# Kernel optimization log

Measured on AMD Instinct MI355X. Metric: run time of the kernel, lower is better.

The kernel has to match this reference:

```python
import jax, jax.numpy as jnp
import numpy as np

NUM_CLASS = 20
STRIDE = 4.0
B, H, W, G, NV = 8, 128, 128, 64, 40


def setup_inputs() -> dict:
    key = jax.random.key(0)
    ks = jax.random.split(key, 8)
    keypoints = jax.random.normal(ks[0], (B, H, W, NUM_CLASS), jnp.float32)
    preg = jax.random.uniform(ks[1], (B, H, W, 4), jnp.float32, 1.0, 40.0)
    fpn = jax.random.normal(ks[2], (B, H, W, NUM_CLASS), jnp.float32)
    masks = jnp.ones((B, H, W, G), jnp.float32)
    scalar_y = jax.random.uniform(ks[3], (B, G), jnp.float32, 5.0, 25.0)
    scalar_x = jax.random.uniform(ks[4], (B, G), jnp.float32, 5.0, 25.0)
    # ground truth: [cy, cx, y1, x1, y2, x2, class]; rows >= NV are zero padding
    rng = np.random.default_rng(0)
    gt = np.zeros((B, G, 7), np.float32)
    cy = rng.uniform(20.0, 492.0, (B, NV)).astype(np.float32)
    cx = rng.uniform(20.0, 492.0, (B, NV)).astype(np.float32)
    hh = rng.uniform(16.0, 120.0, (B, NV)).astype(np.float32)
    ww = rng.uniform(16.0, 120.0, (B, NV)).astype(np.float32)
    gt[:, :NV, 0] = cy
    gt[:, :NV, 1] = cx
    gt[:, :NV, 2] = np.clip(cy - hh / 2, 1.0, 510.0)
    gt[:, :NV, 3] = np.clip(cx - ww / 2, 1.0, 510.0)
    gt[:, :NV, 4] = np.clip(cy + hh / 2, 1.0, 510.0)
    gt[:, :NV, 5] = np.clip(cx + ww / 2, 1.0, 510.0)
    gt[:, :NV, 6] = rng.integers(1, NUM_CLASS + 1, (B, NV)).astype(np.float32)
    return {
        "keypoints": keypoints,
        "preg": preg,
        "fpn": fpn,
        "ground_truth": jnp.asarray(gt),
        "masks": masks,
        "scalar_y": scalar_y,
        "scalar_x": scalar_x,
    }


def _image_loss(gravity_pred, dist_pred, heatmap_pred, gt, masks, sy, sx):
    f32 = jnp.float32
    Hh, Ww, C = gravity_pred.shape
    Gg = gt.shape[0]
    # padding boundary: first row whose cy (col 0) is the minimum (==0 padding)
    slice_index = jnp.argmin(gt[:, 0])
    valid = jnp.arange(Gg) < slice_index
    vf = valid.astype(f32)

    gy = (gt[:, 0] + 0.5) / STRIDE
    gx = (gt[:, 1] + 0.5) / STRIDE
    by1 = (gt[:, 2] + 0.5) / STRIDE
    bx1 = (gt[:, 3] + 0.5) / STRIDE
    by2 = (gt[:, 4] + 0.5) / STRIDE
    bx2 = (gt[:, 5] + 0.5) / STRIDE
    cid = gt[:, 6].astype(jnp.int32) - 1
    kp_y = jnp.clip(jnp.floor(gt[:, 0] / STRIDE).astype(jnp.int32), 0, Hh - 1)
    kp_x = jnp.clip(jnp.floor(gt[:, 1] / STRIDE).astype(jnp.int32), 0, Ww - 1)

    grid_y = (jnp.arange(Hh, dtype=f32) + 0.5)[:, None, None]  # [H,1,1]
    grid_x = (jnp.arange(Ww, dtype=f32) + 0.5)[None, :, None]  # [1,W,1]

    dist_l = grid_x - bx1  # [1,W,G]
    dist_r = bx2 - grid_x
    dist_t = grid_y - by1  # [H,1,G]
    dist_b = by2 - grid_y
    ymask = (dist_t > 0.0).astype(f32) * (dist_b > 0.0).astype(f32)
    xmask = (dist_l > 0.0).astype(f32) * (dist_r > 0.0).astype(f32)
    heatmask = ymask * xmask * masks * vf  # [H,W,G]
    dist_l = dist_l * heatmask
    dist_r = dist_r * heatmask
    dist_t = dist_t * heatmask
    dist_b = dist_b * heatmask
    loc = jnp.max(heatmask, axis=-1)  # [H,W]
    dist_area = (dist_l + dist_r) * (dist_t + dist_b)
    area_pad = dist_area + (1.0 - heatmask) * 1e8
    area_min = jnp.min(area_pad, axis=-1, keepdims=True)
    dist_mask = (dist_area == area_min).astype(f32) * loc[..., None]  # [H,W,G]
    dl = jnp.max(dist_l * dist_mask, axis=-1)
    dr = jnp.max(dist_r * dist_mask, axis=-1)
    dt = jnp.max(dist_t * dist_mask, axis=-1)
    db = jnp.max(dist_b * dist_mask, axis=-1)

    pl, pr, pt, pb = (dist_pred[..., k] for k in range(4))
    inter = (jnp.minimum(dl, pl) + jnp.minimum(dr, pr)) * (jnp.minimum(dt, pt) + jnp.minimum(db, pb))
    union = (dl + dr) * (dt + db) + (pl + pr) * (pt + pb) - inter
    iou = inter / (union + 1e-12)

    red = jnp.exp(-(((grid_y - 0.5 - jnp.floor(gy)) / jnp.sqrt(sy)) ** 2
                    + ((grid_x - 0.5 - jnp.floor(gx)) / jnp.sqrt(sx)) ** 2) / 2.0) * vf  # [H,W,G]
    iou_red = jnp.max(red, axis=-1)
    iou_loss = jnp.sum(-jnp.log(iou + 1e-12) * loc * (iou_red * 4.0 + 1.0))

    # per-class max over gts of that class (== boolean_mask + reduce_max; empty -> 0)
    seg = jnp.where(valid & (cid >= 0) & (cid < C), cid, C)
    red_gt = jnp.maximum(jax.ops.segment_max(red.transpose(2, 0, 1), seg, num_segments=C + 1)[:C], 0.0).transpose(1, 2, 0)
    hm_gt = jnp.maximum(jax.ops.segment_max(dist_mask.transpose(2, 0, 1), seg, num_segments=C + 1)[:C], 0.0).transpose(1, 2, 0)
    gt_kp = jnp.zeros((Hh, Ww, C + 1), f32).at[kp_y, kp_x, seg].max(vf)[..., :C]

    sig, ls = jax.nn.sigmoid, jax.nn.log_sigmoid
    pos = -(1.0 - sig(gravity_pred)) ** 2 * ls(gravity_pred) * gt_kp
    neg = -(1.0 - red_gt) ** 4 * sig(gravity_pred) ** 2 * (-gravity_pred + ls(gravity_pred)) * (1.0 - gt_kp)
    gravity_loss = jnp.sum(pos) + jnp.sum(neg)

    hpos = -10.0 * (1.0 - sig(heatmap_pred)) ** 2 * ls(heatmap_pred) * hm_gt
    hneg = -10.0 * sig(heatmap_pred) ** 2 * (-heatmap_pred + ls(heatmap_pred)) * (1.0 - hm_gt)
    s_hg = jnp.sum(hm_gt)
    hm_loss = jnp.sum(hneg) / (jnp.asarray(Hh * Ww * C, f32) - s_hg)

    cond = s_hg != 0.0
    safe_hg = jnp.where(cond, s_hg, 1.0)
    s_loc = jnp.sum(loc)
    safe_loc = jnp.where(s_loc > 0.0, s_loc, 1.0)
    n_valid = jnp.maximum(slice_index.astype(f32), 1.0)
    hm2 = hm_loss + jnp.sum(hpos) / safe_hg
    iou_out = jnp.where(cond, iou_loss / safe_loc, 0.0)
    grav_out = jnp.where(cond, gravity_loss / n_valid, 0.0)
    hm_out = jnp.where(cond, hm2, hm_loss)
    total = jnp.where(cond, iou_out + grav_out + hm2, hm_loss)
    return iou_out, hm_out, grav_out, total


def reference(keypoints, preg, fpn, ground_truth, masks, scalar_y, scalar_x):
    losses = jax.vmap(_image_loss)(keypoints, preg, fpn, ground_truth, masks, scalar_y, scalar_x)
    # layer returns the mean total loss over the batch
    return jnp.mean(losses[3])
```

## Files before the change

### kernel.cpp

```cpp
#include <hip/hip_runtime.h>
#include <math.h>

#define Bc 8
#define Hc 128
#define Wc 128
#define Cc 20
#define Gc 64
#define HWc (Hc*Wc)
#define NBLK (Bc*HWc/256)

#define WS_STRIDE 768
#define OFF_BOX   0
#define OFF_RED   256
#define OFF_KPIX  512
#define OFF_SEG   576
#define OFF_START 640
#define WS_NV     704
#define WS_ACC    705
#define WS_SLICE  712

__global__ __launch_bounds__(64) void prep_kernel(
    const float* __restrict__ gt, const float* __restrict__ sy,
    const float* __restrict__ sx, float* __restrict__ ws)
{
  const int b = blockIdx.x;
  const int g = threadIdx.x;
  const float* row = gt + (size_t)(b*Gc + g)*7;
  const float cy = row[0];
  const float cx = row[1];

  float v = cy; int idx = g;
  #pragma unroll
  for (int o = 32; o > 0; o >>= 1) {
    const float ov = __shfl_down(v, o, 64);
    const int   oi = __shfl_down(idx, o, 64);
    if (ov < v || (ov == v && oi < idx)) { v = ov; idx = oi; }
  }
  const int slice = __shfl(idx, 0, 64);
  const bool valid = g < slice;
  const int cid = (int)row[6] - 1;
  const int cls = (cid >= 0 && cid < Cc) ? cid : Cc;

  __shared__ int counts[Cc+1], offs[Cc+1], starts[Cc+2];
  if (g < Cc+1) { counts[g] = 0; offs[g] = 0; }
  __syncthreads();
  if (valid) atomicAdd(&counts[cls], 1);
  __syncthreads();
  if (g == 0) {
    int acc = 0;
    for (int c = 0; c < Cc+1; ++c) { starts[c] = acc; acc += counts[c]; }
    starts[Cc+1] = acc;
  }
  __syncthreads();

  float* wb = ws + (size_t)b*WS_STRIDE;
  int*  wbi = (int*)wb;
  float4 bx;
  bx.x = (row[2]+0.5f)*0.25f;
  bx.y = (row[3]+0.5f)*0.25f;
  bx.z = (row[4]+0.5f)*0.25f;
  bx.w = (row[5]+0.5f)*0.25f;
  ((float4*)(wb + OFF_BOX))[g] = bx;
  wbi[OFF_SEG+g] = (valid && cls < Cc) ? cls : Cc;
  if (valid) {
    const int pos = starts[cls] + atomicAdd(&offs[cls], 1);
    float4 rp;
    rp.x = floorf((cy+0.5f)*0.25f);
    rp.y = floorf((cx+0.5f)*0.25f);
    rp.z = 0.5f / sy[b*Gc+g];
    rp.w = 0.5f / sx[b*Gc+g];
    ((float4*)(wb + OFF_RED))[pos] = rp;
    int kpy = (int)floorf(cy*0.25f); kpy = kpy < 0 ? 0 : (kpy > Hc-1 ? Hc-1 : kpy);
    int kpx = (int)floorf(cx*0.25f); kpx = kpx < 0 ? 0 : (kpx > Wc-1 ? Wc-1 : kpx);
    wbi[OFF_KPIX+pos] = kpy*Wc + kpx;
  }
  if (g < Cc+2) wbi[OFF_START+g] = starts[g];
  if (g == 0) { wb[WS_NV] = fmaxf((float)slice, 1.0f); wbi[WS_SLICE] = slice; }
  if (g < 6) wb[WS_ACC+g] = 0.0f;
}

__device__ __forceinline__ float wave_sum(float v) {
  #pragma unroll
  for (int o = 32; o > 0; o >>= 1) v += __shfl_down(v, o, 64);
  return v;
}

__global__ __launch_bounds__(256, 4) void main_kernel(
  const float* __restrict__ kpt, const float* __restrict__ preg,
  const float* __restrict__ fpn, const float* __restrict__ masks,
  const float* __restrict__ wsc, float* __restrict__ wsa)
{
  __shared__ float s_part[4][6];

  const int tid = threadIdx.x;
  const int b   = blockIdx.x >> 6;
  const int pix = blockIdx.x*256 + tid;
  const int hw  = pix & (HWc-1);
  const int h = hw >> 7, w = hw & (Wc-1);

  const float* wb  = wsc + (size_t)b*WS_STRIDE;
  const int*   wbi = (const int*)wb;
  const float4* __restrict__ box4 = (const float4*)(wb + OFF_BOX);
  const float4* __restrict__ red4 = (const float4*)(wb + OFF_RED);
  const int nslice = wbi[WS_SLICE];

  const float wx = w + 0.5f, hy = h + 0.5f;
  const float px_ = (float)w, py_ = (float)h;
  const float4* mrow4 = (const float4*)(masks + (size_t)pix*Gc);

  float amin = 3.0e38f; float loc = 0.0f, mmin = 0.0f; int gmin = 0;
  const int nfull = nslice & ~7;
  float4 ma = mrow4[0], mb = mrow4[1];
  for (int g0 = 0; g0 < nfull; g0 += 8) {
    const int pf = (g0 + 8) < Gc ? ((g0 + 8) >> 2) : 14;
    const float4 na = mrow4[pf];
    const float4 nb = mrow4[pf + 1];
    #pragma unroll
    for (int j = 0; j < 8; ++j) {
      const int g = g0 + j;
      const float m = (j==0)?ma.x:(j==1)?ma.y:(j==2)?ma.z:(j==3)?ma.w
                    : (j==4)?mb.x:(j==5)?mb.y:(j==6)?mb.z:mb.w;
      const float4 bx = box4[g];
      const float dl = wx - bx.y, dr = bx.w - wx;
      const float dt = hy - bx.x, db = bx.z - hy;
      const bool inb = (dl > 0.f) & (dr > 0.f) & (dt > 0.f) & (db > 0.f);
      const float hm = inb ? m : 0.f;
      const float area = (dl*hm + dr*hm) * (dt*hm + db*hm);
      const float ap = area + (1.f - hm)*1e8f;
      if (ap < amin) { amin = ap; gmin = g; mmin = m; }
      loc = fmaxf(loc, hm);
    }
    ma = na; mb = nb;
  }
  for (int g = nfull; g < nslice; ++g) {
    const float m = masks[(size_t)pix*Gc + g];
    const float4 bx = box4[g];
    const float dl = wx - bx.y, dr = bx.w - wx;
    const float dt = hy - bx.x, db = bx.z - hy;
    const bool inb = (dl > 0.f) & (dr > 0.f) & (dt > 0.f) & (db > 0.f);
    const float hm = inb ? m : 0.f;
    const float area = (dl*hm + dr*hm) * (dt*hm + db*hm);
    const float ap = area + (1.f - hm)*1e8f;
    if (ap < amin) { amin = ap; gmin = g; mmin = m; }
    loc = fmaxf(loc, hm);
  }

  float dlm=0.f, drm=0.f, dtm=0.f, dbm=0.f, hmval=0.f; int cmin = Cc;
  if (loc > 0.f) {
    const float4 bx = box4[gmin];
    const float dl = wx - bx.y, dr = bx.w - wx;
    const float dt = hy - bx.x, db = bx.z - hy;
    const float area = (dl*mmin + dr*mmin) * (dt*mmin + db*mmin);
    if (area == amin) {
      dlm = dl*mmin*loc; drm = dr*mmin*loc; dtm = dt*mmin*loc; dbm = db*mmin*loc;
      cmin = wbi[OFF_SEG + gmin];
      hmval = loc;
    }
  }

  const float4* kq4 = (const float4*)(kpt + (size_t)pix*Cc);
  const float4* fq4 = (const float4*)(fpn + (size_t)pix*Cc);
  float4 kcur = kq4[0], fcur = fq4[0];
  float gargmax = -1e30f, grav = 0.f, hneg = 0.f;
  int sb = wbi[OFF_START];
  for (int cg = 0; cg < 5; ++cg) {
    const int nx = cg < 4 ? cg + 1 : 4;
    const float4 knxt = kq4[nx];
    const float4 fnxt = fq4[nx];
    #pragma unroll
    for (int j = 0; j < 4; ++j) {
      const int c = cg*4 + j;
      const int s1 = wbi[OFF_START + c + 1];
      float ramax = -1e30f; bool kpv = false;
      for (int i = sb; i < s1; ++i) {
        const float4 rp = red4[i];
        const int kpix = wbi[OFF_KPIX + i];
        const float dy = py_ - rp.x, dx = px_ - rp.y;
        const float arg = -(dy*dy*rp.z + dx*dx*rp.w);
        ramax = fmaxf(ramax, arg);
        kpv = kpv | (kpix == hw);
      }
      sb = s1;
      const float rmax = __expf(ramax);
      gargmax = fmaxf(gargmax, ramax);
      const float x  = (j==0)?kcur.x:(j==1)?kcur.y:(j==2)?kcur.z:kcur.w;
      const float e  = __expf(-fabsf(x));
      const float t  = 1.f + e;
      const float r  = 1.f / t;
      const float L  = __logf(t);
      const float s  = (x >= 0.f) ? r : e*r;
      const float lsx = fminf(x, 0.f) - L;
      const float kv = kpv ? 1.f : 0.f;
      const float om = 1.f - rmax;
      const float om4 = (om*om)*(om*om);
      const float oms = 1.f - s;
      grav += (-(oms*oms)*lsx)*kv + (-om4*(s*s)*(lsx - x))*(1.f - kv);

      const float fx  = (j==0)?fcur.x:(j==1)?fcur.y:(j==2)?fcur.z:fcur.w;
      const float ef  = __expf(-fabsf(fx));
      const float tf  = 1.f + ef;
      const float rf  = 1.f / tf;
      const float Lf  = __logf(tf);
      const float sf  = (fx >= 0.f) ? rf : ef*rf;
      const float lsf = fminf(fx, 0.f) - Lf;
      hneg += -10.f*(sf*sf)*(lsf - fx);
    }
    kcur = knxt; fcur = fnxt;
  }
  {
    const int e20 = wbi[OFF_START + Cc + 1];
    for (int i = sb; i < e20; ++i) {
      const float4 rp = red4[i];
      const float dy = py_ - rp.x, dx = px_ - rp.y;
      gargmax = fmaxf(gargmax, -(dy*dy*rp.z + dx*dx*rp.w));
    }
  }
  const float iou_red = __expf(gargmax);

  const float4 p4 = *(const float4*)(preg + (size_t)pix*4);
  const float inter = (fminf(dlm,p4.x)+fminf(drm,p4.y)) * (fminf(dtm,p4.z)+fminf(dbm,p4.w));
  const float uni = (dlm+drm)*(dtm+dbm) + (p4.x+p4.y)*(p4.z+p4.w) - inter;
  const float iou = inter / (uni + 1e-12f);
  const float t_iou = -__logf(iou + 1e-12f) * loc * (iou_red*4.f + 1.f);

  float hpos = 0.f, shg = 0.f;
  if (hmval > 0.f && cmin < Cc) {
    const float fx  = fpn[(size_t)pix*Cc + cmin];
    const float ef  = __expf(-fabsf(fx));
    const float tf  = 1.f + ef;
    const float rf  = 1.f / tf;
    const float Lf  = __logf(tf);
    const float sf  = (fx >= 0.f) ? rf : ef*rf;
    const float lsf = fminf(fx, 0.f) - Lf;
    const float osf = 1.f - sf;
    hpos = -10.f*(osf*osf)*lsf*hmval;
    hneg -= (-10.f*(sf*sf)*(lsf - fx))*hmval;
    shg = hmval;
  }

  float v0 = wave_sum(t_iou);
  float v1 = wave_sum(loc);
  float v2 = wave_sum(grav);
  float v3 = wave_sum(hpos);
  float v4 = wave_sum(hneg);
  float v5 = wave_sum(shg);
  const int wv = tid >> 6, ln = tid & 63;
  if (ln == 0) {
    s_part[wv][0]=v0; s_part[wv][1]=v1; s_part[wv][2]=v2;
    s_part[wv][3]=v3; s_part[wv][4]=v4; s_part[wv][5]=v5;
  }
  __syncthreads();
  if (tid < 6) {
    const float a = s_part[0][tid] + s_part[1][tid] + s_part[2][tid] + s_part[3][tid];
    atomicAdd(wsa + (size_t)b*WS_STRIDE + WS_ACC + tid, a);
  }
}

__global__ __launch_bounds__(64) void fin_kernel(const float* __restrict__ ws,
                                                 float* __restrict__ out)
{
  const int b = threadIdx.x;
  float total = 0.0f;
  if (b < Bc) {
    const float* wb = ws + (size_t)b*WS_STRIDE;
    const float iou_loss = wb[WS_ACC+0];
    const float s_loc    = wb[WS_ACC+1];
    const float grav     = wb[WS_ACC+2];
    const float hposs    = wb[WS_ACC+3];
    const float hnegs    = wb[WS_ACC+4];
    const float shg      = wb[WS_ACC+5];
    const float nv       = wb[WS_NV];
    const float hm_loss  = hnegs / ((float)(HWc*Cc) - shg);
    const bool  cond     = (shg != 0.0f);
    const float safe_hg  = cond ? shg : 1.0f;
    const float safe_loc = (s_loc > 0.0f) ? s_loc : 1.0f;
    const float hm2      = hm_loss + hposs/safe_hg;
    total = cond ? (iou_loss/safe_loc + grav/nv + hm2) : hm_loss;
  }
  #pragma unroll
  for (int o = 4; o > 0; o >>= 1) total += __shfl_down(total, o, 64);
  if (b == 0) out[0] = total * (1.0f/(float)Bc);
}

extern "C" void kernel_launch(void* const* d_in, const int* in_sizes, int n_in,
                              void* d_out, int out_size, void* d_ws, size_t ws_size,
                              hipStream_t stream) {
  const float* kpt  = (const float*)d_in[0];
  const float* preg = (const float*)d_in[1];
  const float* fpn  = (const float*)d_in[2];
  const float* gt   = (const float*)d_in[3];
  const float* mk   = (const float*)d_in[4];
  const float* sy   = (const float*)d_in[5];
  const float* sx   = (const float*)d_in[6];
  float* ws  = (float*)d_ws;
  float* out = (float*)d_out;

  prep_kernel<<<Bc, 64, 0, stream>>>(gt, sy, sx, ws);
  main_kernel<<<NBLK, 256, 0, stream>>>(kpt, preg, fpn, mk, ws, ws);
  fin_kernel<<<1, 64, 0, stream>>>(ws, out);
}
```

Baseline: 116.6 us.

## Fuse prep into main kernel, stage inputs via coalesced LDS transposes, drop atomics

Removes the separate prep kernel: each main block recomputes the per-image GT slice, class buckets and gaussian parameters in shared memory. Keypoint, fpn and mask rows are loaded with coalesced block-wide float4 reads and transposed through LDS, with masks streamed in 16-group chunks and the next chunk prefetched into registers. Per-block partial sums are written to the workspace and reduced in a widened final kernel instead of using global atomics. This costs about 45KB of LDS per block, lowers the occupancy hint to 2, adds extra barriers, and repeats the GT prep work in every block.

```diff
diff --git a/kernel.cpp b/kernel.cpp
--- a/kernel.cpp
+++ b/kernel.cpp
@@ -9,75 +9,6 @@
 #define HWc (Hc*Wc)
 #define NBLK (Bc*HWc/256)
 
-#define WS_STRIDE 768
-#define OFF_BOX   0
-#define OFF_RED   256
-#define OFF_KPIX  512
-#define OFF_SEG   576
-#define OFF_START 640
-#define WS_NV     704
-#define WS_ACC    705
-#define WS_SLICE  712
-
-__global__ __launch_bounds__(64) void prep_kernel(
-    const float* __restrict__ gt, const float* __restrict__ sy,
-    const float* __restrict__ sx, float* __restrict__ ws)
-{
-  const int b = blockIdx.x;
-  const int g = threadIdx.x;
-  const float* row = gt + (size_t)(b*Gc + g)*7;
-  const float cy = row[0];
-  const float cx = row[1];
-
-  float v = cy; int idx = g;
-  #pragma unroll
-  for (int o = 32; o > 0; o >>= 1) {
-    const float ov = __shfl_down(v, o, 64);
-    const int   oi = __shfl_down(idx, o, 64);
-    if (ov < v || (ov == v && oi < idx)) { v = ov; idx = oi; }
-  }
-  const int slice = __shfl(idx, 0, 64);
-  const bool valid = g < slice;
-  const int cid = (int)row[6] - 1;
-  const int cls = (cid >= 0 && cid < Cc) ? cid : Cc;
-
-  __shared__ int counts[Cc+1], offs[Cc+1], starts[Cc+2];
-  if (g < Cc+1) { counts[g] = 0; offs[g] = 0; }
-  __syncthreads();
-  if (valid) atomicAdd(&counts[cls], 1);
-  __syncthreads();
-  if (g == 0) {
-    int acc = 0;
-    for (int c = 0; c < Cc+1; ++c) { starts[c] = acc; acc += counts[c]; }
-    starts[Cc+1] = acc;
-  }
-  __syncthreads();
-
-  float* wb = ws + (size_t)b*WS_STRIDE;
-  int*  wbi = (int*)wb;
-  float4 bx;
-  bx.x = (row[2]+0.5f)*0.25f;
-  bx.y = (row[3]+0.5f)*0.25f;
-  bx.z = (row[4]+0.5f)*0.25f;
-  bx.w = (row[5]+0.5f)*0.25f;
-  ((float4*)(wb + OFF_BOX))[g] = bx;
-  wbi[OFF_SEG+g] = (valid && cls < Cc) ? cls : Cc;
-  if (valid) {
-    const int pos = starts[cls] + atomicAdd(&offs[cls], 1);
-    float4 rp;
-    rp.x = floorf((cy+0.5f)*0.25f);
-    rp.y = floorf((cx+0.5f)*0.25f);
-    rp.z = 0.5f / sy[b*Gc+g];
-    rp.w = 0.5f / sx[b*Gc+g];
-    ((float4*)(wb + OFF_RED))[pos] = rp;
-    int kpy = (int)floorf(cy*0.25f); kpy = kpy < 0 ? 0 : (kpy > Hc-1 ? Hc-1 : kpy);
-    int kpx = (int)floorf(cx*0.25f); kpx = kpx < 0 ? 0 : (kpx > Wc-1 ? Wc-1 : kpx);
-    wbi[OFF_KPIX+pos] = kpy*Wc + kpx;
-  }
-  if (g < Cc+2) wbi[OFF_START+g] = starts[g];
-  if (g == 0) { wb[WS_NV] = fmaxf((float)slice, 1.0f); wbi[WS_SLICE] = slice; }
-  if (g < 6) wb[WS_ACC+g] = 0.0f;
-}
 
 __device__ __forceinline__ float wave_sum(float v) {
   #pragma unroll
@@ -85,44 +16,128 @@
   return v;
 }
 
-__global__ __launch_bounds__(256, 4) void main_kernel(
-  const float* __restrict__ kpt, const float* __restrict__ preg,
-  const float* __restrict__ fpn, const float* __restrict__ masks,
-  const float* __restrict__ wsc, float* __restrict__ wsa)
+__global__ __launch_bounds__(256, 2) void main_kernel(
+    const float* __restrict__ kpt, const float* __restrict__ preg,
+    const float* __restrict__ fpn, const float* __restrict__ masks,
+    const float* __restrict__ gt,  const float* __restrict__ sy,
+    const float* __restrict__ sx,  float* __restrict__ ws)
 {
+  __shared__ float s_kpt[Cc*256];
+  __shared__ float s_fpn[Cc*256];
+  __shared__ float s_masks[16*256];
+  __shared__ float4 s_red[Gc];
+  __shared__ int s_kpix[Gc];
+  __shared__ int s_seg[Gc];
+  __shared__ int s_starts[Cc+2];
+  __shared__ int s_counts[Cc+1];
+  __shared__ int s_offs[Cc+1];
+  __shared__ int s_nslice;
   __shared__ float s_part[4][6];
 
-  const int tid = threadIdx.x;
-  const int b   = blockIdx.x >> 6;
-  const int pix = blockIdx.x*256 + tid;
-  const int hw  = pix & (HWc-1);
+  const int T = threadIdx.x;
+  const int b = blockIdx.x >> 6;
+  const int pixbase = blockIdx.x * 256;
+  const int pix = pixbase + T;
+  const int hw = pix & (HWc-1);
   const int h = hw >> 7, w = hw & (Wc-1);
 
-  const float* wb  = wsc + (size_t)b*WS_STRIDE;
-  const int*   wbi = (const int*)wb;
-  const float4* __restrict__ box4 = (const float4*)(wb + OFF_BOX);
-  const float4* __restrict__ red4 = (const float4*)(wb + OFF_RED);
-  const int nslice = wbi[WS_SLICE];
+  const float4* __restrict__ kg4 = (const float4*)(kpt + (size_t)pixbase*Cc);
+  const float4* __restrict__ fg4 = (const float4*)(fpn + (size_t)pixbase*Cc);
+  const float4* __restrict__ mg4 = (const float4*)(masks + (size_t)pixbase*Gc);
+  float4 kpr[5], fpr[5], mpr[4];
+  #pragma unroll
+  for (int k = 0; k < 5; ++k) { kpr[k] = kg4[T + 256*k]; fpr[k] = fg4[T + 256*k]; }
+  #pragma unroll
+  for (int k = 0; k < 4; ++k) mpr[k] = mg4[((T>>2) + 64*k)*16 + (T&3)];
+
+  if (T < Cc+1) { s_counts[T] = 0; s_offs[T] = 0; }
+  float cy = 0.f, cx = 0.f; int cls = Cc; bool valid = false;
+  if (T < 64) {
+    const float* grow = gt + (size_t)(b*Gc + T)*7;
+    cy = grow[0]; cx = grow[1];
+    float v = cy; int idx = T;
+    #pragma unroll
+    for (int o = 32; o > 0; o >>= 1) {
+      const float ov = __shfl_down(v, o, 64);
+      const int   oi = __shfl_down(idx, o, 64);
+      if (ov < v || (ov == v && oi < idx)) { v = ov; idx = oi; }
+    }
+    const int slice = __shfl(idx, 0, 64);
+    const int cid = (int)grow[6] - 1;
+    cls = (cid >= 0 && cid < Cc) ? cid : Cc;
+    valid = T < slice;
+    s_seg[T] = (valid && cls < Cc) ? cls : Cc;
+    if (T == 0) s_nslice = slice;
+  }
+  __syncthreads();
+  if (T < 64 && valid) atomicAdd(&s_counts[cls], 1);
+  __syncthreads();
+  if (T == 0) {
+    int acc = 0;
+    #pragma unroll
+    for (int c = 0; c < Cc+1; ++c) { s_starts[c] = acc; acc += s_counts[c]; }
+    s_starts[Cc+1] = acc;
+  }
+  __syncthreads();
+  if (T < 64 && valid) {
+    const int pos = s_starts[cls] + atomicAdd(&s_offs[cls], 1);
+    float4 rp;
+    rp.x = floorf((cy + 0.5f)*0.25f);
+    rp.y = floorf((cx + 0.5f)*0.25f);
+    rp.z = 0.5f / sy[b*Gc + T];
+    rp.w = 0.5f / sx[b*Gc + T];
+    s_red[pos] = rp;
+    int kpy = (int)floorf(cy*0.25f); kpy = kpy < 0 ? 0 : (kpy > Hc-1 ? Hc-1 : kpy);
+    int kpx = (int)floorf(cx*0.25f); kpx = kpx < 0 ? 0 : (kpx > Wc-1 ? Wc-1 : kpx);
+    s_kpix[pos] = kpy*Wc + kpx;
+  }
+
+  #pragma unroll
+  for (int k = 0; k < 5; ++k) {
+    const int base = (T + 256*k)*4;
+    const float ke[4] = {kpr[k].x, kpr[k].y, kpr[k].z, kpr[k].w};
+    const float fe[4] = {fpr[k].x, fpr[k].y, fpr[k].z, fpr[k].w};
+    #pragma unroll
+    for (int i = 0; i < 4; ++i) {
+      const int li = base + i;
+      const int p = li / 20;
+      const int c = li - p*20;
+      s_kpt[c*256 + p] = ke[i];
+      s_fpn[c*256 + p] = fe[i];
+    }
+  }
+  #pragma unroll
+  for (int k = 0; k < 4; ++k) {
+    const int p  = (T>>2) + 64*k;
+    const int g0 = (T&3)*4;
+    const float me[4] = {mpr[k].x, mpr[k].y, mpr[k].z, mpr[k].w};
+    #pragma unroll
+    for (int i = 0; i < 4; ++i) s_masks[(g0+i)*256 + p] = me[i];
+  }
+  #pragma unroll
+  for (int k = 0; k < 4; ++k) mpr[k] = mg4[((T>>2) + 64*k)*16 + 4 + (T&3)];
+  __syncthreads();
+
+  const int nslice = s_nslice;
+  const int nch = (nslice + 15) >> 4;
 
   const float wx = w + 0.5f, hy = h + 0.5f;
+  const float wxp = wx - 0.125f, wxm = 0.125f - wx;
+  const float hyp = hy - 0.125f, hym = 0.125f - hy;
   const float px_ = (float)w, py_ = (float)h;
-  const float4* mrow4 = (const float4*)(masks + (size_t)pix*Gc);
-
-  float amin = 3.0e38f; float loc = 0.0f, mmin = 0.0f; int gmin = 0;
-  const int nfull = nslice & ~7;
-  float4 ma = mrow4[0], mb = mrow4[1];
-  for (int g0 = 0; g0 < nfull; g0 += 8) {
-    const int pf = (g0 + 8) < Gc ? ((g0 + 8) >> 2) : 14;
-    const float4 na = mrow4[pf];
-    const float4 nb = mrow4[pf + 1];
-    #pragma unroll
-    for (int j = 0; j < 8; ++j) {
-      const int g = g0 + j;
-      const float m = (j==0)?ma.x:(j==1)?ma.y:(j==2)?ma.z:(j==3)?ma.w
-                    : (j==4)?mb.x:(j==5)?mb.y:(j==6)?mb.z:mb.w;
-      const float4 bx = box4[g];
-      const float dl = wx - bx.y, dr = bx.w - wx;
-      const float dt = hy - bx.x, db = bx.z - hy;
+
+  float amin = 3.0e38f, loc = 0.f, mmin = 0.f; int gmin = 0;
+  for (int cc = 0; cc < nch; ++cc) {
+    const int rem = nslice - cc*16;
+    const int gend = rem < 16 ? rem : 16;
+    for (int gl = 0; gl < gend; ++gl) {
+      const int g = cc*16 + gl;
+      const float* grow = gt + (size_t)(b*Gc + g)*7;
+      const float m = s_masks[gl*256 + T];
+      const float dl = fmaf(-0.25f, grow[3], wxp);
+      const float dr = fmaf( 0.25f, grow[5], wxm);
+      const float dt = fmaf(-0.25f, grow[2], hyp);
+      const float db = fmaf( 0.25f, grow[4], hym);
       const bool inb = (dl > 0.f) & (dr > 0.f) & (dt > 0.f) & (db > 0.f);
       const float hm = inb ? m : 0.f;
       const float area = (dl*hm + dr*hm) * (dt*hm + db*hm);
@@ -130,87 +145,83 @@
       if (ap < amin) { amin = ap; gmin = g; mmin = m; }
       loc = fmaxf(loc, hm);
     }
-    ma = na; mb = nb;
-  }
-  for (int g = nfull; g < nslice; ++g) {
-    const float m = masks[(size_t)pix*Gc + g];
-    const float4 bx = box4[g];
-    const float dl = wx - bx.y, dr = bx.w - wx;
-    const float dt = hy - bx.x, db = bx.z - hy;
-    const bool inb = (dl > 0.f) & (dr > 0.f) & (dt > 0.f) & (db > 0.f);
-    const float hm = inb ? m : 0.f;
-    const float area = (dl*hm + dr*hm) * (dt*hm + db*hm);
-    const float ap = area + (1.f - hm)*1e8f;
-    if (ap < amin) { amin = ap; gmin = g; mmin = m; }
-    loc = fmaxf(loc, hm);
+    if (cc + 1 < nch) {
+      __syncthreads();
+      #pragma unroll
+      for (int k = 0; k < 4; ++k) {
+        const int p  = (T>>2) + 64*k;
+        const int g0 = (T&3)*4;
+        const float me[4] = {mpr[k].x, mpr[k].y, mpr[k].z, mpr[k].w};
+        #pragma unroll
+        for (int i = 0; i < 4; ++i) s_masks[(g0+i)*256 + p] = me[i];
+      }
+      if (cc + 2 < nch) {
+        #pragma unroll
+        for (int k = 0; k < 4; ++k)
+          mpr[k] = mg4[((T>>2) + 64*k)*16 + (cc+2)*4 + (T&3)];
+      }
+      __syncthreads();
+    }
   }
 
   float dlm=0.f, drm=0.f, dtm=0.f, dbm=0.f, hmval=0.f; int cmin = Cc;
   if (loc > 0.f) {
-    const float4 bx = box4[gmin];
-    const float dl = wx - bx.y, dr = bx.w - wx;
-    const float dt = hy - bx.x, db = bx.z - hy;
+    const float* gr = gt + (size_t)(b*Gc + gmin)*7;
+    const float dl = fmaf(-0.25f, gr[3], wxp);
+    const float dr = fmaf( 0.25f, gr[5], wxm);
+    const float dt = fmaf(-0.25f, gr[2], hyp);
+    const float db = fmaf( 0.25f, gr[4], hym);
     const float area = (dl*mmin + dr*mmin) * (dt*mmin + db*mmin);
     if (area == amin) {
       dlm = dl*mmin*loc; drm = dr*mmin*loc; dtm = dt*mmin*loc; dbm = db*mmin*loc;
-      cmin = wbi[OFF_SEG + gmin];
+      cmin = s_seg[gmin];
       hmval = loc;
     }
   }
 
-  const float4* kq4 = (const float4*)(kpt + (size_t)pix*Cc);
-  const float4* fq4 = (const float4*)(fpn + (size_t)pix*Cc);
-  float4 kcur = kq4[0], fcur = fq4[0];
   float gargmax = -1e30f, grav = 0.f, hneg = 0.f;
-  int sb = wbi[OFF_START];
-  for (int cg = 0; cg < 5; ++cg) {
-    const int nx = cg < 4 ? cg + 1 : 4;
-    const float4 knxt = kq4[nx];
-    const float4 fnxt = fq4[nx];
-    #pragma unroll
-    for (int j = 0; j < 4; ++j) {
-      const int c = cg*4 + j;
-      const int s1 = wbi[OFF_START + c + 1];
-      float ramax = -1e30f; bool kpv = false;
-      for (int i = sb; i < s1; ++i) {
-        const float4 rp = red4[i];
-        const int kpix = wbi[OFF_KPIX + i];
-        const float dy = py_ - rp.x, dx = px_ - rp.y;
-        const float arg = -(dy*dy*rp.z + dx*dx*rp.w);
-        ramax = fmaxf(ramax, arg);
-        kpv = kpv | (kpix == hw);
-      }
-      sb = s1;
-      const float rmax = __expf(ramax);
-      gargmax = fmaxf(gargmax, ramax);
-      const float x  = (j==0)?kcur.x:(j==1)?kcur.y:(j==2)?kcur.z:kcur.w;
-      const float e  = __expf(-fabsf(x));
-      const float t  = 1.f + e;
-      const float r  = 1.f / t;
-      const float L  = __logf(t);
-      const float s  = (x >= 0.f) ? r : e*r;
-      const float lsx = fminf(x, 0.f) - L;
-      const float kv = kpv ? 1.f : 0.f;
-      const float om = 1.f - rmax;
-      const float om4 = (om*om)*(om*om);
-      const float oms = 1.f - s;
-      grav += (-(oms*oms)*lsx)*kv + (-om4*(s*s)*(lsx - x))*(1.f - kv);
-
-      const float fx  = (j==0)?fcur.x:(j==1)?fcur.y:(j==2)?fcur.z:fcur.w;
-      const float ef  = __expf(-fabsf(fx));
-      const float tf  = 1.f + ef;
-      const float rf  = 1.f / tf;
-      const float Lf  = __logf(tf);
-      const float sf  = (fx >= 0.f) ? rf : ef*rf;
-      const float lsf = fminf(fx, 0.f) - Lf;
-      hneg += -10.f*(sf*sf)*(lsf - fx);
-    }
-    kcur = knxt; fcur = fnxt;
+  int sb = s_starts[0];
+  for (int c = 0; c < Cc; ++c) {
+    const int s1 = s_starts[c+1];
+    float ramax = -1e30f; bool kpv = false;
+    for (int i = sb; i < s1; ++i) {
+      const float4 rp = s_red[i];
+      const int kpix = s_kpix[i];
+      const float dy = py_ - rp.x, dx = px_ - rp.y;
+      const float arg = -(dy*dy*rp.z + dx*dx*rp.w);
+      ramax = fmaxf(ramax, arg);
+      kpv = kpv | (kpix == hw);
+    }
+    sb = s1;
+    const float rmax = __expf(ramax);
+    gargmax = fmaxf(gargmax, ramax);
+
+    const float x  = s_kpt[c*256 + T];
+    const float e  = __expf(-fabsf(x));
+    const float t  = 1.f + e;
+    const float r  = 1.f / t;
+    const float Lt = __logf(t);
+    const float s  = (x >= 0.f) ? r : e*r;
+    const float lsx = fminf(x, 0.f) - Lt;
+    const float kv = kpv ? 1.f : 0.f;
+    const float om = 1.f - rmax;
+    const float om4 = (om*om)*(om*om);
+    const float oms = 1.f - s;
+    grav += (-(oms*oms)*lsx)*kv + (-om4*(s*s)*(lsx - x))*(1.f - kv);
+
+    const float fx  = s_fpn[c*256 + T];
+    const float ef  = __expf(-fabsf(fx));
+    const float tf  = 1.f + ef;
+    const float rf  = 1.f / tf;
+    const float Lf  = __logf(tf);
+    const float sf  = (fx >= 0.f) ? rf : ef*rf;
+    const float lsf = fminf(fx, 0.f) - Lf;
+    hneg += -10.f*(sf*sf)*(lsf - fx);
   }
   {
-    const int e20 = wbi[OFF_START + Cc + 1];
+    const int e20 = s_starts[Cc+1];
     for (int i = sb; i < e20; ++i) {
-      const float4 rp = red4[i];
+      const float4 rp = s_red[i];
       const float dy = py_ - rp.x, dx = px_ - rp.y;
       gargmax = fmaxf(gargmax, -(dy*dy*rp.z + dx*dx*rp.w));
     }
@@ -225,7 +236,7 @@
 
   float hpos = 0.f, shg = 0.f;
   if (hmval > 0.f && cmin < Cc) {
-    const float fx  = fpn[(size_t)pix*Cc + cmin];
+    const float fx  = s_fpn[cmin*256 + T];
     const float ef  = __expf(-fabsf(fx));
     const float tf  = 1.f + ef;
     const float rf  = 1.f / tf;
@@ -244,42 +255,59 @@
   float v3 = wave_sum(hpos);
   float v4 = wave_sum(hneg);
   float v5 = wave_sum(shg);
-  const int wv = tid >> 6, ln = tid & 63;
+  const int wv = T >> 6, ln = T & 63;
   if (ln == 0) {
     s_part[wv][0]=v0; s_part[wv][1]=v1; s_part[wv][2]=v2;
     s_part[wv][3]=v3; s_part[wv][4]=v4; s_part[wv][5]=v5;
   }
   __syncthreads();
-  if (tid < 6) {
-    const float a = s_part[0][tid] + s_part[1][tid] + s_part[2][tid] + s_part[3][tid];
-    atomicAdd(wsa + (size_t)b*WS_STRIDE + WS_ACC + tid, a);
-  }
+  if (T < 6)
+    ws[(size_t)blockIdx.x*8 + T] =
+        s_part[0][T] + s_part[1][T] + s_part[2][T] + s_part[3][T];
 }
 
-__global__ __launch_bounds__(64) void fin_kernel(const float* __restrict__ ws,
-                                                 float* __restrict__ out)
+__global__ __launch_bounds__(256) void fin_kernel(
+    const float* __restrict__ gt, const float* __restrict__ ws,
+    float* __restrict__ out)
 {
-  const int b = threadIdx.x;
-  float total = 0.0f;
-  if (b < Bc) {
-    const float* wb = ws + (size_t)b*WS_STRIDE;
-    const float iou_loss = wb[WS_ACC+0];
-    const float s_loc    = wb[WS_ACC+1];
-    const float grav     = wb[WS_ACC+2];
-    const float hposs    = wb[WS_ACC+3];
-    const float hnegs    = wb[WS_ACC+4];
-    const float shg      = wb[WS_ACC+5];
-    const float nv       = wb[WS_NV];
-    const float hm_loss  = hnegs / ((float)(HWc*Cc) - shg);
-    const bool  cond     = (shg != 0.0f);
-    const float safe_hg  = cond ? shg : 1.0f;
-    const float safe_loc = (s_loc > 0.0f) ? s_loc : 1.0f;
-    const float hm2      = hm_loss + hposs/safe_hg;
-    total = cond ? (iou_loss/safe_loc + grav/nv + hm2) : hm_loss;
-  }
-  #pragma unroll
-  for (int o = 4; o > 0; o >>= 1) total += __shfl_down(total, o, 64);
-  if (b == 0) out[0] = total * (1.0f/(float)Bc);
+  const int T = threadIdx.x, wv = T >> 6, ln = T & 63;
+  __shared__ float s_tot[Bc];
+  #pragma unroll
+  for (int rep = 0; rep < 2; ++rep) {
+    const int b = wv + 4*rep;
+    const float cy = gt[(size_t)(b*Gc + ln)*7];
+    float v = cy; int idx = ln;
+    #pragma unroll
+    for (int o = 32; o > 0; o >>= 1) {
+      const float ov = __shfl_down(v, o, 64);
+      const int   oi = __shfl_down(idx, o, 64);
+      if (ov < v || (ov == v && oi < idx)) { v = ov; idx = oi; }
+    }
+    const int slice = __shfl(idx, 0, 64);
+    const float* pb = ws + (size_t)(b*64 + ln)*8;
+    const float a0 = wave_sum(pb[0]);
+    const float a1 = wave_sum(pb[1]);
+    const float a2 = wave_sum(pb[2]);
+    const float a3 = wave_sum(pb[3]);
+    const float a4 = wave_sum(pb[4]);
+    const float a5 = wave_sum(pb[5]);
+    if (ln == 0) {
+      const float nv       = fmaxf((float)slice, 1.0f);
+      const float hm_loss  = a4 / ((float)(HWc*Cc) - a5);
+      const bool  cond     = (a5 != 0.0f);
+      const float safe_hg  = cond ? a5 : 1.0f;
+      const float safe_loc = (a1 > 0.0f) ? a1 : 1.0f;
+      const float hm2      = hm_loss + a3/safe_hg;
+      s_tot[b] = cond ? (a0/safe_loc + a2/nv + hm2) : hm_loss;
+    }
+  }
+  __syncthreads();
+  if (T == 0) {
+    float s = 0.f;
+    #pragma unroll
+    for (int i = 0; i < Bc; ++i) s += s_tot[i];
+    out[0] = s * (1.0f/(float)Bc);
+  }
 }
 
 extern "C" void kernel_launch(void* const* d_in, const int* in_sizes, int n_in,
@@ -295,7 +323,6 @@
   float* ws  = (float*)d_ws;
   float* out = (float*)d_out;
 
-  prep_kernel<<<Bc, 64, 0, stream>>>(gt, sy, sx, ws);
-  main_kernel<<<NBLK, 256, 0, stream>>>(kpt, preg, fpn, mk, ws, ws);
-  fin_kernel<<<1, 64, 0, stream>>>(ws, out);
+  main_kernel<<<NBLK, 256, 0, stream>>>(kpt, preg, fpn, mk, gt, sy, sx, ws);
+  fin_kernel<<<1, 256, 0, stream>>>(ws ? gt : gt, ws, out);
 }
```

Result: slower. 120.7 us (+3.5%).

## Split each pixel's work across two lanes with shuffle-merged reductions

Applied to the files above, without the earlier changes.

Each pixel is now handled by two lanes in the same wave, doubling the thread count. The lanes interleave mask groups, box checks and class channels, then merge argmin, max and gargmax results with xor shuffles. The goal is more memory-level parallelism and shorter per-thread serial loops on the memory-bound mask and keypoint reads. The cost is duplicated box work at the end, extra shuffles, and redundant preg loads on both halves.

```diff
diff --git a/kernel.cpp b/kernel.cpp
--- a/kernel.cpp
+++ b/kernel.cpp
@@ -7,7 +7,7 @@
 #define Cc 20
 #define Gc 64
 #define HWc (Hc*Wc)
-#define NBLK (Bc*HWc/256)
+#define NBLK2 (Bc*HWc/128)
 
 #define WS_STRIDE 768
 #define OFF_BOX   0
@@ -93,8 +93,11 @@
   __shared__ float s_part[4][6];
 
   const int tid = threadIdx.x;
-  const int b   = blockIdx.x >> 6;
-  const int pix = blockIdx.x*256 + tid;
+  const int wv = tid >> 6, ln = tid & 63;
+  const int half = ln >> 5, sub = ln & 31;
+  const int pi  = wv*32 + sub;
+  const int pix = blockIdx.x*128 + pi;
+  const int b   = blockIdx.x >> 7;
   const int hw  = pix & (HWc-1);
   const int h = hw >> 7, w = hw & (Wc-1);
 
@@ -108,41 +111,46 @@
   const float px_ = (float)w, py_ = (float)h;
   const float4* mrow4 = (const float4*)(masks + (size_t)pix*Gc);
 
-  float amin = 3.0e38f; float loc = 0.0f, mmin = 0.0f; int gmin = 0;
-  const int nfull = nslice & ~7;
-  float4 ma = mrow4[0], mb = mrow4[1];
-  for (int g0 = 0; g0 < nfull; g0 += 8) {
-    const int pf = (g0 + 8) < Gc ? ((g0 + 8) >> 2) : 14;
-    const float4 na = mrow4[pf];
-    const float4 nb = mrow4[pf + 1];
+  const float4 p4 = *(const float4*)(preg + (size_t)pix*4);
+  const float4* kq4 = (const float4*)(kpt + (size_t)pix*Cc);
+  const float4* fq4 = (const float4*)(fpn + (size_t)pix*Cc);
+  const float4 kg0 = kq4[half], kg1 = kq4[2+half], kg2 = kq4[4];
+  const float4 fg0 = fq4[half], fg1 = fq4[2+half], fg2 = fq4[4];
+
+  float amin = 3.0e38f, loc = 0.f, mmin = 0.f; int gmin = 0;
+  const int nC2 = (nslice + 7) >> 3;
+  float4 mc0 = mrow4[half];
+  float4 mc1 = mrow4[2 + half];
+  for (int c2 = 0; c2 < nC2; ++c2) {
+    const int pfci = 2*(c2+2) + half;
+    const float4 mn = mrow4[pfci < 16 ? pfci : (14+half)];
+    const int ci = 2*c2 + half;
     #pragma unroll
-    for (int j = 0; j < 8; ++j) {
-      const int g = g0 + j;
-      const float m = (j==0)?ma.x:(j==1)?ma.y:(j==2)?ma.z:(j==3)?ma.w
-                    : (j==4)?mb.x:(j==5)?mb.y:(j==6)?mb.z:mb.w;
+    for (int j = 0; j < 4; ++j) {
+      const int g = ci*4 + j;
+      const float m = (j==0)?mc0.x:(j==1)?mc0.y:(j==2)?mc0.z:mc0.w;
       const float4 bx = box4[g];
       const float dl = wx - bx.y, dr = bx.w - wx;
       const float dt = hy - bx.x, db = bx.z - hy;
-      const bool inb = (dl > 0.f) & (dr > 0.f) & (dt > 0.f) & (db > 0.f);
+      const bool inb = (dl > 0.f) & (dr > 0.f) & (dt > 0.f) & (db > 0.f)
+                       & (g < nslice);
       const float hm = inb ? m : 0.f;
       const float area = (dl*hm + dr*hm) * (dt*hm + db*hm);
       const float ap = area + (1.f - hm)*1e8f;
       if (ap < amin) { amin = ap; gmin = g; mmin = m; }
       loc = fmaxf(loc, hm);
     }
-    ma = na; mb = nb;
-  }
-  for (int g = nfull; g < nslice; ++g) {
-    const float m = masks[(size_t)pix*Gc + g];
-    const float4 bx = box4[g];
-    const float dl = wx - bx.y, dr = bx.w - wx;
-    const float dt = hy - bx.x, db = bx.z - hy;
-    const bool inb = (dl > 0.f) & (dr > 0.f) & (dt > 0.f) & (db > 0.f);
-    const float hm = inb ? m : 0.f;
-    const float area = (dl*hm + dr*hm) * (dt*hm + db*hm);
-    const float ap = area + (1.f - hm)*1e8f;
-    if (ap < amin) { amin = ap; gmin = g; mmin = m; }
-    loc = fmaxf(loc, hm);
+    mc0 = mc1; mc1 = mn;
+  }
+  {
+    const float o_amin = __shfl_xor(amin, 32, 64);
+    const int   o_gmin = __shfl_xor(gmin, 32, 64);
+    const float o_mmin = __shfl_xor(mmin, 32, 64);
+    const float o_loc  = __shfl_xor(loc , 32, 64);
+    if (o_amin < amin || (o_amin == amin && o_gmin < gmin)) {
+      amin = o_amin; gmin = o_gmin; mmin = o_mmin;
+    }
+    loc = fmaxf(loc, o_loc);
   }
 
   float dlm=0.f, drm=0.f, dtm=0.f, dbm=0.f, hmval=0.f; int cmin = Cc;
@@ -158,21 +166,19 @@
     }
   }
 
-  const float4* kq4 = (const float4*)(kpt + (size_t)pix*Cc);
-  const float4* fq4 = (const float4*)(fpn + (size_t)pix*Cc);
-  float4 kcur = kq4[0], fcur = fq4[0];
   float gargmax = -1e30f, grav = 0.f, hneg = 0.f;
-  int sb = wbi[OFF_START];
-  for (int cg = 0; cg < 5; ++cg) {
-    const int nx = cg < 4 ? cg + 1 : 4;
-    const float4 knxt = kq4[nx];
-    const float4 fnxt = fq4[nx];
+  #pragma unroll
+  for (int grp = 0; grp < 2; ++grp) {
+    const int idx = 2*grp + half;
+    const float4 kq = grp ? kg1 : kg0;
+    const float4 fq = grp ? fg1 : fg0;
     #pragma unroll
     for (int j = 0; j < 4; ++j) {
-      const int c = cg*4 + j;
+      const int c = idx*4 + j;
+      const int s0 = wbi[OFF_START + c];
       const int s1 = wbi[OFF_START + c + 1];
       float ramax = -1e30f; bool kpv = false;
-      for (int i = sb; i < s1; ++i) {
+      for (int i = s0; i < s1; ++i) {
         const float4 rp = red4[i];
         const int kpix = wbi[OFF_KPIX + i];
         const float dy = py_ - rp.x, dx = px_ - rp.y;
@@ -180,10 +186,9 @@
         ramax = fmaxf(ramax, arg);
         kpv = kpv | (kpix == hw);
       }
-      sb = s1;
       const float rmax = __expf(ramax);
       gargmax = fmaxf(gargmax, ramax);
-      const float x  = (j==0)?kcur.x:(j==1)?kcur.y:(j==2)?kcur.z:kcur.w;
+      const float x  = (j==0)?kq.x:(j==1)?kq.y:(j==2)?kq.z:kq.w;
       const float e  = __expf(-fabsf(x));
       const float t  = 1.f + e;
       const float r  = 1.f / t;
@@ -196,7 +201,7 @@
       const float oms = 1.f - s;
       grav += (-(oms*oms)*lsx)*kv + (-om4*(s*s)*(lsx - x))*(1.f - kv);
 
-      const float fx  = (j==0)?fcur.x:(j==1)?fcur.y:(j==2)?fcur.z:fcur.w;
+      const float fx  = (j==0)?fq.x:(j==1)?fq.y:(j==2)?fq.z:fq.w;
       const float ef  = __expf(-fabsf(fx));
       const float tf  = 1.f + ef;
       const float rf  = 1.f / tf;
@@ -205,26 +210,65 @@
       const float lsf = fminf(fx, 0.f) - Lf;
       hneg += -10.f*(sf*sf)*(lsf - fx);
     }
-    kcur = knxt; fcur = fnxt;
-  }
-  {
+  }
+  #pragma unroll
+  for (int j = 0; j < 2; ++j) {
+    const int c = 16 + 2*half + j;
+    const int cp = 2*half + j;
+    const int s0 = wbi[OFF_START + c];
+    const int s1 = wbi[OFF_START + c + 1];
+    float ramax = -1e30f; bool kpv = false;
+    for (int i = s0; i < s1; ++i) {
+      const float4 rp = red4[i];
+      const int kpix = wbi[OFF_KPIX + i];
+      const float dy = py_ - rp.x, dx = px_ - rp.y;
+      const float arg = -(dy*dy*rp.z + dx*dx*rp.w);
+      ramax = fmaxf(ramax, arg);
+      kpv = kpv | (kpix == hw);
+    }
+    const float rmax = __expf(ramax);
+    gargmax = fmaxf(gargmax, ramax);
+    const float x  = (cp==0)?kg2.x:(cp==1)?kg2.y:(cp==2)?kg2.z:kg2.w;
+    const float e  = __expf(-fabsf(x));
+    const float t  = 1.f + e;
+    const float r  = 1.f / t;
+    const float L  = __logf(t);
+    const float s  = (x >= 0.f) ? r : e*r;
+    const float lsx = fminf(x, 0.f) - L;
+    const float kv = kpv ? 1.f : 0.f;
+    const float om = 1.f - rmax;
+    const float om4 = (om*om)*(om*om);
+    const float oms = 1.f - s;
+    grav += (-(oms*oms)*lsx)*kv + (-om4*(s*s)*(lsx - x))*(1.f - kv);
+
+    const float fx  = (cp==0)?fg2.x:(cp==1)?fg2.y:(cp==2)?fg2.z:fg2.w;
+    const float ef  = __expf(-fabsf(fx));
+    const float tf  = 1.f + ef;
+    const float rf  = 1.f / tf;
+    const float Lf  = __logf(tf);
+    const float sf  = (fx >= 0.f) ? rf : ef*rf;
+    const float lsf = fminf(fx, 0.f) - Lf;
+    hneg += -10.f*(sf*sf)*(lsf - fx);
+  }
+  if (half) {
+    const int s0  = wbi[OFF_START + Cc];
     const int e20 = wbi[OFF_START + Cc + 1];
-    for (int i = sb; i < e20; ++i) {
+    for (int i = s0; i < e20; ++i) {
       const float4 rp = red4[i];
       const float dy = py_ - rp.x, dx = px_ - rp.y;
       gargmax = fmaxf(gargmax, -(dy*dy*rp.z + dx*dx*rp.w));
     }
   }
+  gargmax = fmaxf(gargmax, __shfl_xor(gargmax, 32, 64));
   const float iou_red = __expf(gargmax);
 
-  const float4 p4 = *(const float4*)(preg + (size_t)pix*4);
   const float inter = (fminf(dlm,p4.x)+fminf(drm,p4.y)) * (fminf(dtm,p4.z)+fminf(dbm,p4.w));
   const float uni = (dlm+drm)*(dtm+dbm) + (p4.x+p4.y)*(p4.z+p4.w) - inter;
   const float iou = inter / (uni + 1e-12f);
   const float t_iou = -__logf(iou + 1e-12f) * loc * (iou_red*4.f + 1.f);
 
   float hpos = 0.f, shg = 0.f;
-  if (hmval > 0.f && cmin < Cc) {
+  if (half == 0 && hmval > 0.f && cmin < Cc) {
     const float fx  = fpn[(size_t)pix*Cc + cmin];
     const float ef  = __expf(-fabsf(fx));
     const float tf  = 1.f + ef;
@@ -238,13 +282,13 @@
     shg = hmval;
   }
 
-  float v0 = wave_sum(t_iou);
-  float v1 = wave_sum(loc);
+  const float zi = half ? 0.f : 1.f;
+  float v0 = wave_sum(t_iou * zi);
+  float v1 = wave_sum(loc * zi);
   float v2 = wave_sum(grav);
   float v3 = wave_sum(hpos);
   float v4 = wave_sum(hneg);
   float v5 = wave_sum(shg);
-  const int wv = tid >> 6, ln = tid & 63;
   if (ln == 0) {
     s_part[wv][0]=v0; s_part[wv][1]=v1; s_part[wv][2]=v2;
     s_part[wv][3]=v3; s_part[wv][4]=v4; s_part[wv][5]=v5;
@@ -296,6 +340,6 @@
   float* out = (float*)d_out;
 
   prep_kernel<<<Bc, 64, 0, stream>>>(gt, sy, sx, ws);
-  main_kernel<<<NBLK, 256, 0, stream>>>(kpt, preg, fpn, mk, ws, ws);
+  main_kernel<<<NBLK2, 256, 0, stream>>>(kpt, preg, fpn, mk, ws, ws);
   fin_kernel<<<1, 64, 0, stream>>>(ws, out);
 }
```

Result: slower. 119.8 us (+2.7%).
